# Kernel tuning notes

Hardware: AMD Instinct MI355X
Metric: run time of the kernel (lower is better)

## Reference

```python
import jax, jax.numpy as jnp
import numpy as np

N, F_IN, D_IN, D_OUT = 1024, 256, 128, 64  # nodes, raw feat, in_features, out_features


def setup_inputs() -> dict:
    key = jax.random.key(0)
    k_adj, k_x, k_lw, k_w = jax.random.split(key, 4)
    # Random symmetric binary adjacency, avg degree ~32, self-loops on the diagonal
    p = 32.0 / N
    u = jax.random.uniform(k_adj, (N, N))
    A = (u < p).astype(jnp.float32)
    A = jnp.maximum(A, A.T)
    diag = jnp.arange(N)
    A = A.at[diag, diag].set(1.0)
    # --- caculation(): derived masks ---
    A0 = A.at[diag, diag].set(0.0)                 # adjacency without self loops
    sib = A0 @ A0 + A0                             # sibling matrix
    sib = sib.at[diag, diag].set(0.0)
    neighbor_count = jnp.maximum(A0.sum(axis=1, keepdims=True), 1.0)  # [N,1]
    # --- features and parameters ---
    node_features = jax.random.normal(k_x, (N, F_IN), dtype=jnp.float32)
    k_lw1, k_lw2 = jax.random.split(k_lw)
    lin_w = jax.random.normal(k_lw1, (D_IN, F_IN), dtype=jnp.float32) * np.float32(np.sqrt(2.0 / F_IN))
    lin_b = jnp.zeros((D_IN,), dtype=jnp.float32)
    weight = jax.random.normal(k_w, (D_IN, D_OUT), dtype=jnp.float32) * np.float32(np.sqrt(2.0 / D_IN))
    return {
        "node_features": node_features,
        "adjacency_matrix": A,
        "mask_father": A[:, None, :],              # [N,1,N]
        "neighbor_count": neighbor_count,          # [N,1]
        "mask_hadamard": sib[:, None, :],          # [N,1,N]
        "lin_w": lin_w,
        "lin_b": lin_b,
        "weight": weight,
    }


def reference(node_features, adjacency_matrix, mask_father, neighbor_count, mask_hadamard, lin_w, lin_b, weight):
    # Linear projection created inside torch forward: x @ W^T + b
    x = node_features @ lin_w.T + lin_b            # [N, D_IN]
    wf = x @ weight                                # [N, F]  (F = out_features)
    sib = mask_hadamard[:, 0, :]                   # [N, N]
    mf = mask_father[:, 0, :]                      # [N, N]
    # H[b,f,j] = wf[b,f] * wf[j,f] * sib[b,j]   (masked pairwise hadamard, [N,F,N])
    H = wf[:, :, None] * wf.T[None, :, :] * sib[:, None, :]
    # S[i,f,j] = sum_b A[i,b] * H[b,f,j]        (batched adjacency matmul)
    S = jnp.einsum('ib,bfj->ifj', adjacency_matrix, H)
    # mask by father adjacency, sum over j, normalize by neighbor_count^2
    out = (S * mf[:, None, :]).sum(axis=2) / (neighbor_count ** 2)   # [N, F]
    return out
```

## Files before the change

### kernel.cpp

```cpp
#include <hip/hip_runtime.h>

#define N 1024
#define F_IN 256
#define D_IN 128
#define D_OUT 64
#define KMAX 128

__global__ __launch_bounds__(256) void w2_kernel(
    const float* __restrict__ lin_w, const float* __restrict__ lin_b,
    const float* __restrict__ weight, float* __restrict__ W2,
    float* __restrict__ b2)
{
    const int t = threadIdx.x;
    if (blockIdx.x < 64) {
        const int k = blockIdx.x * 4 + (t >> 6);
        const int f = t & 63;
        float acc = 0.0f;
        #pragma unroll 4
        for (int d = 0; d < D_IN; ++d)
            acc += lin_w[d * F_IN + k] * weight[d * D_OUT + f];
        W2[k * D_OUT + f] = acc;
    } else if (t < D_OUT) {
        float acc = 0.0f;
        #pragma unroll 4
        for (int d = 0; d < D_IN; ++d)
            acc += lin_b[d] * weight[d * D_OUT + t];
        b2[t] = acc;
    }
}

__global__ __launch_bounds__(256) void wf2_kernel(
    const float* __restrict__ nf, const float* __restrict__ W2,
    const float* __restrict__ b2, float* __restrict__ wf)
{
    const int t = threadIdx.x;
    const int i = blockIdx.x * 4 + (t >> 6);
    const int f = t & 63;
    const float4* nf4 = (const float4*)(nf + (size_t)i * F_IN);
    float acc = b2[f];
    #pragma unroll 4
    for (int kk = 0; kk < F_IN / 4; ++kk) {
        const float4 v = nf4[kk];
        const float* w = W2 + kk * 4 * D_OUT + f;
        acc += v.x * w[0] + v.y * w[D_OUT] + v.z * w[2 * D_OUT] + v.w * w[3 * D_OUT];
    }
    wf[(size_t)i * D_OUT + f] = acc;
}

__global__ __launch_bounds__(1024, 8) void pair_kernel(
    const float* __restrict__ A, const float* __restrict__ sib,
    const float* __restrict__ nc, const float* __restrict__ wf,
    float* __restrict__ out)
{
    __shared__ float         wf_s[KMAX * D_OUT];
    __shared__ unsigned char sib_s[KMAX * KMAX];
    __shared__ int           nbr[KMAX];
    __shared__ int           cnt;
    __shared__ float         red[16 * D_OUT];

    const int i = blockIdx.x, t = threadIdx.x;
    const int wave = t >> 6, lane = t & 63;
    if (t == 0) cnt = 0;
    __syncthreads();

    {
        const float a = A[(size_t)i * N + t];
        if (a != 0.0f) {
            int p = atomicAdd(&cnt, 1);
            if (p < KMAX) nbr[p] = t;
        }
    }
    __syncthreads();
    int K = cnt; if (K > KMAX) K = KMAX;

    for (int idx = t; idx < K * (D_OUT / 4); idx += 1024)
        ((float4*)wf_s)[idx] = ((const float4*)wf)[nbr[idx >> 4] * (D_OUT / 4) + (idx & 15)];

    for (int bi = wave; bi < K; bi += 16) {
        const float* srow = sib + (size_t)nbr[bi] * N;
        for (int j = lane; j < K; j += 64)
            sib_s[bi * KMAX + j] = (unsigned char)(srow[nbr[j]] + 0.5f);
    }
    __syncthreads();

    float acc = 0.0f;
    for (int bi = wave; bi < K; bi += 16) {
        const float wb = wf_s[bi * D_OUT + lane];
        const unsigned char* sr = sib_s + bi * KMAX;
        #pragma unroll 4
        for (int j = bi + 1; j < K; ++j) {
            acc += (float)sr[j] * wb * wf_s[j * D_OUT + lane];
        }
    }
    red[wave * D_OUT + lane] = acc;
    __syncthreads();

    if (t < D_OUT) {
        float v = 0.0f;
        #pragma unroll
        for (int w = 0; w < 16; ++w) v += red[w * D_OUT + t];
        const float c = nc[i];
        out[(size_t)i * D_OUT + t] = 2.0f * v / (c * c);
    }
}

extern "C" void kernel_launch(void* const* d_in, const int* in_sizes, int n_in,
                              void* d_out, int out_size, void* d_ws, size_t ws_size,
                              hipStream_t stream) {
    const float* nf     = (const float*)d_in[0];
    const float* A      = (const float*)d_in[1];
    const float* nc     = (const float*)d_in[3];
    const float* sib    = (const float*)d_in[4];
    const float* lin_w  = (const float*)d_in[5];
    const float* lin_b  = (const float*)d_in[6];
    const float* weight = (const float*)d_in[7];
    float*       out    = (float*)d_out;

    float* wf = (float*)d_ws;
    float* W2 = wf + (size_t)N * D_OUT;
    float* b2 = W2 + (size_t)F_IN * D_OUT;

    w2_kernel <<<65,  256,  0, stream>>>(lin_w, lin_b, weight, W2, b2);
    wf2_kernel<<<N/4, 256,  0, stream>>>(nf, W2, b2, wf);
    pair_kernel<<<N,  1024, 0, stream>>>(A, sib, nc, wf, out);
}
```

Baseline: 127.2 us.

## Precompute byte sibling mask and neighbor lists in prep kernel; vectorize pair loop

Adds a prep kernel that turns the float sibling matrix into bytes and builds per-row neighbor lists with ballot compaction. The pair kernel then gathers from the byte matrix instead of doing scattered float reads, and its inner loop uses float4 accumulators split across four j-lanes with a shuffle reduction. The wf projection kernel splits the K dimension across two waves. The prep kernel still reads the full sib and A matrices and adds a launch. K is now capped at 124, which could change results for very high-degree rows.

```diff
diff --git a/kernel.cpp b/kernel.cpp
--- a/kernel.cpp
+++ b/kernel.cpp
@@ -5,6 +5,46 @@
 #define D_IN 128
 #define D_OUT 64
 #define KMAX 128
+
+__global__ __launch_bounds__(256) void prep_kernel(
+    const float* __restrict__ A, const float* __restrict__ sib,
+    unsigned char* __restrict__ sib8, unsigned short* __restrict__ nbrg,
+    int* __restrict__ cntg)
+{
+    const int i = blockIdx.x, t = threadIdx.x;
+    const int lane = t & 63, wave = t >> 6;
+
+    {
+        const float4 v = ((const float4*)(sib + (size_t)i * N))[t];
+        uchar4 u;
+        u.x = (unsigned char)(v.x + 0.5f);
+        u.y = (unsigned char)(v.y + 0.5f);
+        u.z = (unsigned char)(v.z + 0.5f);
+        u.w = (unsigned char)(v.w + 0.5f);
+        ((uchar4*)(sib8 + (size_t)i * N))[t] = u;
+    }
+
+    __shared__ int woff[4];
+    __shared__ int base;
+    if (t == 0) base = 0;
+    const float* arow = A + (size_t)i * N;
+    for (int c = 0; c < 4; ++c) {
+        __syncthreads();
+        const int j = c * 256 + t;
+        const float a = arow[j];
+        const unsigned long long m = __ballot(a != 0.0f);
+        if (lane == 0) woff[wave] = __popcll(m);
+        __syncthreads();
+        int off = base;
+        for (int w = 0; w < wave; ++w) off += woff[w];
+        const int pos = off + __popcll(m & ((1ULL << lane) - 1ULL));
+        if (a != 0.0f && pos < KMAX) nbrg[(size_t)i * KMAX + pos] = (unsigned short)j;
+        __syncthreads();
+        if (t == 0) base += woff[0] + woff[1] + woff[2] + woff[3];
+    }
+    __syncthreads();
+    if (t == 0) cntg[i] = base < KMAX ? base : KMAX;
+}
 
 __global__ __launch_bounds__(256) void w2_kernel(
     const float* __restrict__ lin_w, const float* __restrict__ lin_b,
@@ -33,70 +73,85 @@
     const float* __restrict__ nf, const float* __restrict__ W2,
     const float* __restrict__ b2, float* __restrict__ wf)
 {
-    const int t = threadIdx.x;
-    const int i = blockIdx.x * 4 + (t >> 6);
-    const int f = t & 63;
-    const float4* nf4 = (const float4*)(nf + (size_t)i * F_IN);
-    float acc = b2[f];
-    #pragma unroll 4
-    for (int kk = 0; kk < F_IN / 4; ++kk) {
+    __shared__ float red[4 * D_OUT];
+    const int t = threadIdx.x, lane = t & 63, wave = t >> 6;
+    const int row = blockIdx.x * 2 + (wave >> 1);
+    const int half = wave & 1;
+    const float4* nf4 = (const float4*)(nf + (size_t)row * F_IN);
+    float acc = half ? 0.0f : b2[lane];
+    #pragma unroll 8
+    for (int kk = half * 32; kk < half * 32 + 32; ++kk) {
         const float4 v = nf4[kk];
-        const float* w = W2 + kk * 4 * D_OUT + f;
+        const float* w = W2 + kk * 4 * D_OUT + lane;
         acc += v.x * w[0] + v.y * w[D_OUT] + v.z * w[2 * D_OUT] + v.w * w[3 * D_OUT];
     }
-    wf[(size_t)i * D_OUT + f] = acc;
+    red[wave * D_OUT + lane] = acc;
+    __syncthreads();
+    if (t < 128) {
+        const int rr = t >> 6, f = t & 63;
+        wf[(size_t)(blockIdx.x * 2 + rr) * D_OUT + f] =
+            red[(rr * 2) * D_OUT + f] + red[(rr * 2 + 1) * D_OUT + f];
+    }
 }
 
-__global__ __launch_bounds__(1024, 8) void pair_kernel(
-    const float* __restrict__ A, const float* __restrict__ sib,
-    const float* __restrict__ nc, const float* __restrict__ wf,
-    float* __restrict__ out)
+__global__ __launch_bounds__(1024, 8) void pair2_kernel(
+    const unsigned char* __restrict__ sib8, const unsigned short* __restrict__ nbrg,
+    const int* __restrict__ cntg, const float* __restrict__ nc,
+    const float* __restrict__ wf, float* __restrict__ out)
 {
-    __shared__ float         wf_s[KMAX * D_OUT];
-    __shared__ unsigned char sib_s[KMAX * KMAX];
-    __shared__ int           nbr[KMAX];
-    __shared__ int           cnt;
-    __shared__ float         red[16 * D_OUT];
+    __shared__ float          wf_s[(KMAX + 4) * D_OUT];
+    __shared__ unsigned char  sib_s[KMAX * KMAX];
+    __shared__ unsigned short nbr[KMAX];
+    __shared__ float          red[16 * D_OUT];
 
     const int i = blockIdx.x, t = threadIdx.x;
     const int wave = t >> 6, lane = t & 63;
-    if (t == 0) cnt = 0;
+    int K = cntg[i]; if (K > 124) K = 124;
+
+    ((int*)sib_s)[t]        = 0;
+    ((int*)sib_s)[t + 1024] = 0;
+    ((int*)sib_s)[t + 2048] = 0;
+    ((int*)sib_s)[t + 3072] = 0;
+    if (t < 256) wf_s[K * D_OUT + t] = 0.0f;
+    if (t < KMAX) nbr[t] = nbrg[(size_t)i * KMAX + t];
     __syncthreads();
 
-    {
-        const float a = A[(size_t)i * N + t];
-        if (a != 0.0f) {
-            int p = atomicAdd(&cnt, 1);
-            if (p < KMAX) nbr[p] = t;
-        }
-    }
-    __syncthreads();
-    int K = cnt; if (K > KMAX) K = KMAX;
-
     for (int idx = t; idx < K * (D_OUT / 4); idx += 1024)
-        ((float4*)wf_s)[idx] = ((const float4*)wf)[nbr[idx >> 4] * (D_OUT / 4) + (idx & 15)];
-
-    for (int bi = wave; bi < K; bi += 16) {
-        const float* srow = sib + (size_t)nbr[bi] * N;
-        for (int j = lane; j < K; j += 64)
-            sib_s[bi * KMAX + j] = (unsigned char)(srow[nbr[j]] + 0.5f);
+        ((float4*)wf_s)[idx] =
+            ((const float4*)wf)[(int)nbr[idx >> 4] * (D_OUT / 4) + (idx & 15)];
+    for (int idx = t; idx < K * KMAX; idx += 1024) {
+        const int bi = idx >> 7, j = idx & (KMAX - 1);
+        if (j < K) sib_s[idx] = sib8[(size_t)nbr[bi] * N + nbr[j]];
     }
     __syncthreads();
 
-    float acc = 0.0f;
+    const int f4 = (lane & 15) * 4, p = lane >> 4;
+    float4 acc = make_float4(0.f, 0.f, 0.f, 0.f);
     for (int bi = wave; bi < K; bi += 16) {
-        const float wb = wf_s[bi * D_OUT + lane];
+        const float4 wb = *(const float4*)&wf_s[bi * D_OUT + f4];
         const unsigned char* sr = sib_s + bi * KMAX;
-        #pragma unroll 4
-        for (int j = bi + 1; j < K; ++j) {
-            acc += (float)sr[j] * wb * wf_s[j * D_OUT + lane];
+        for (int j0 = bi + 1; j0 < K; j0 += 4) {
+            const int j = j0 + p;
+            const float s = (float)sr[j];
+            const float4 wj = *(const float4*)&wf_s[j * D_OUT + f4];
+            acc.x += s * (wb.x * wj.x);
+            acc.y += s * (wb.y * wj.y);
+            acc.z += s * (wb.z * wj.z);
+            acc.w += s * (wb.w * wj.w);
         }
     }
-    red[wave * D_OUT + lane] = acc;
+    #pragma unroll
+    for (int m = 16; m <= 32; m += m) {
+        acc.x += __shfl_xor(acc.x, m, 64);
+        acc.y += __shfl_xor(acc.y, m, 64);
+        acc.z += __shfl_xor(acc.z, m, 64);
+        acc.w += __shfl_xor(acc.w, m, 64);
+    }
+    if (p == 0) *(float4*)&red[wave * D_OUT + f4] = acc;
     __syncthreads();
 
     if (t < D_OUT) {
-        float v = 0.0f;
+        float v = 0.f;
         #pragma unroll
         for (int w = 0; w < 16; ++w) v += red[w * D_OUT + t];
         const float c = nc[i];
@@ -116,11 +171,16 @@
     const float* weight = (const float*)d_in[7];
     float*       out    = (float*)d_out;
 
-    float* wf = (float*)d_ws;
-    float* W2 = wf + (size_t)N * D_OUT;
-    float* b2 = W2 + (size_t)F_IN * D_OUT;
+    char* ws = (char*)d_ws;
+    float*          wf    = (float*)(ws);
+    float*          W2    = (float*)(ws + 262144);
+    float*          b2    = (float*)(ws + 327680);
+    unsigned char*  sib8  = (unsigned char*)(ws + 328704);
+    unsigned short* nbr16 = (unsigned short*)(ws + 1377280);
+    int*            cnt   = (int*)(ws + 1639424);
 
-    w2_kernel <<<65,  256,  0, stream>>>(lin_w, lin_b, weight, W2, b2);
-    wf2_kernel<<<N/4, 256,  0, stream>>>(nf, W2, b2, wf);
-    pair_kernel<<<N,  1024, 0, stream>>>(A, sib, nc, wf, out);
+    prep_kernel<<<N,   256,  0, stream>>>(A, sib, sib8, nbr16, cnt);
+    w2_kernel  <<<65,  256,  0, stream>>>(lin_w, lin_b, weight, W2, b2);
+    wf2_kernel <<<N/2, 256,  0, stream>>>(nf, W2, b2, wf);
+    pair2_kernel<<<N,  1024, 0, stream>>>(sib8, nbr16, cnt, nc, wf, out);
 }
```

Result: faster. 118.9 us (-6.5%).
